# Kernel tuning notes

Hardware: AMD Instinct MI355X
Metric: run time of the kernel (lower is better)

Reference implementation:

```python
import jax, jax.numpy as jnp
import numpy as np

N_NODES = 100000
N_EDGES = 3200000
IN_CH = 256


def setup_inputs() -> dict:
    key = jax.random.key(0)
    ks = jax.random.split(key, 8)
    x = jax.random.normal(ks[0], (N_NODES, IN_CH), dtype=jnp.float32)
    edge_index = jax.random.randint(ks[1], (2, N_EDGES), 0, N_NODES, dtype=jnp.int64)
    alpha = jnp.ones((), dtype=jnp.float32)
    beta = jnp.ones((), dtype=jnp.float32)
    s = 1.0 / np.sqrt(IN_CH)
    W_mlp = jax.random.normal(ks[2], (1, IN_CH), dtype=jnp.float32) * s
    W_lin = jax.random.normal(ks[3], (1, IN_CH), dtype=jnp.float32) * s
    W_gcn = jax.random.normal(ks[4], (1, IN_CH), dtype=jnp.float32) * s
    W_att = jax.random.normal(ks[5], (3, 3), dtype=jnp.float32) * (1.0 / np.sqrt(3))
    b_att = jax.random.normal(ks[6], (3,), dtype=jnp.float32) * 0.1
    return {"x": x, "edge_index": edge_index, "alpha": alpha, "beta": beta,
            "W_mlp": W_mlp, "W_lin": W_lin, "W_gcn": W_gcn,
            "W_att": W_att, "b_att": b_att}


def _gcn_conv(x, edge_index, W_gcn, num_nodes):
    # PyG GCNConv: add self-loops, symmetric normalization, no bias.
    loop = jnp.arange(num_nodes, dtype=edge_index.dtype)
    row = jnp.concatenate([edge_index[0], loop])  # source
    col = jnp.concatenate([edge_index[1], loop])  # target
    deg = jax.ops.segment_sum(jnp.ones_like(col, dtype=x.dtype), col,
                              num_segments=num_nodes)
    dinv = jnp.where(deg > 0, jax.lax.rsqrt(deg), 0.0)
    norm = dinv[row] * dinv[col]                  # [E+N]
    xw = x @ W_gcn.T                               # [N, 1]
    msg = norm[:, None] * xw[row]                  # [E+N, 1]
    return jax.ops.segment_sum(msg, col, num_segments=num_nodes)  # [N, 1]


def reference(x, edge_index, alpha, beta, W_mlp, W_lin, W_gcn, W_att, b_att):
    num_nodes = x.shape[0]
    # score1: in-degree based
    deg = jax.ops.segment_sum(jnp.ones((edge_index.shape[1],), dtype=x.dtype),
                              edge_index[1], num_segments=num_nodes)
    score1 = jax.nn.sigmoid(alpha * jnp.sqrt(deg) + beta)           # [N]
    # score2: tiny MLP
    score2 = jax.nn.sigmoid((x @ W_mlp.T)[:, 0])                    # [N]
    # score3: GCNConv + linear
    gcn_out = _gcn_conv(x, edge_index, W_gcn, num_nodes)            # [N,1]
    score3 = jax.nn.sigmoid((gcn_out + x @ W_lin.T)[:, 0])          # [N]
    scores = jnp.stack([score1, score2, score3], axis=1)            # [N,3]
    weight = jax.nn.softmax(scores @ W_att.T + b_att, axis=1)       # [N,3]
    fitness = jnp.sum(weight * scores, axis=1)                      # [N]
    return fitness
```

## Files before the change

kernel.cpp:

```cpp
#include <hip/hip_runtime.h>
#include <math.h>

#define N_CH    256
#define SBSHIFT 11
#define SBN     2048
#define NSMAX   64
#define CH      4096


__device__ __forceinline__ float sigmoidf_(float v) {
    return 1.0f / (1.0f + expf(-v));
}

__device__ __forceinline__ void build_tables(const int* sbT, int ns,
                                             int* sbsL, int* cstL) {
    if (threadIdx.x == 0) {
        int run = 0, c = 0;
        for (int i = 0; i < ns; ++i) {
            sbsL[i] = run;
            cstL[i] = c;
            int len = sbT[i];
            run += len;
            c += (len + CH - 1) / CH;
        }
        sbsL[ns] = run;
        cstL[ns] = c;
    }
}

__global__ __launch_bounds__(256) void hist_kernel(
    const int* __restrict__ dst, int* __restrict__ H1,
    int n_edges, int ns, int nch)
{
    __shared__ int h8[NSMAX * 8];
    int c = blockIdx.x;
    for (int i = threadIdx.x; i < NSMAX * 8; i += 256) h8[i] = 0;
    __syncthreads();
    int copy = (int)threadIdx.x & 7;
    int start = c * CH;
    #pragma unroll
    for (int m = 0; m < 4; ++m) {
        int e = start + (m * 256 + (int)threadIdx.x) * 4;
        if (e + 3 < n_edges) {
            int4 d4 = *(const int4*)(dst + e);
            atomicAdd(&h8[(d4.x >> SBSHIFT) * 8 + copy], 1);
            atomicAdd(&h8[(d4.y >> SBSHIFT) * 8 + copy], 1);
            atomicAdd(&h8[(d4.z >> SBSHIFT) * 8 + copy], 1);
            atomicAdd(&h8[(d4.w >> SBSHIFT) * 8 + copy], 1);
        } else {
            for (int ee = e; ee < n_edges && ee >= 0; ++ee)
                atomicAdd(&h8[(dst[ee] >> SBSHIFT) * 8 + copy], 1);
        }
    }
    __syncthreads();
    if (threadIdx.x < (unsigned)ns) {
        int s = 0;
        #pragma unroll
        for (int k = 0; k < 8; ++k) s += h8[threadIdx.x * 8 + k];
        H1[(size_t)threadIdx.x * nch + c] = s;
    }
}

__global__ __launch_bounds__(1024) void scanA_kernel(
    const int* __restrict__ H1, int* __restrict__ O, int* __restrict__ sbT,
    int nch)
{
    __shared__ int s[1024];
    int sb = blockIdx.x, t = threadIdx.x;
    int v = (t < nch) ? H1[(size_t)sb * nch + t] : 0;
    s[t] = v;
    __syncthreads();
    for (int off = 1; off < 1024; off <<= 1) {
        int a = s[t];
        int b = (t >= off) ? s[t - off] : 0;
        __syncthreads();
        s[t] = a + b;
        __syncthreads();
    }
    if (t < nch) O[(size_t)sb * nch + t] = s[t] - v;
    if (t == 1023) sbT[sb] = s[1023];
}

__global__ __launch_bounds__(256) void scatter_dots_kernel(
    const int* __restrict__ src, const int* __restrict__ dst,
    const int* __restrict__ sbT, const int* __restrict__ O,
    const int* __restrict__ H1, int* __restrict__ cpack,
    const float* __restrict__ x,
    const float* __restrict__ Wmlp, const float* __restrict__ Wlin,
    const float* __restrict__ Wgcn,
    float* __restrict__ s2dot, float* __restrict__ s3lin, float* __restrict__ xw,
    int n_nodes, int n_edges, int ns, int nch)
{
    __shared__ int lp[NSMAX + 1];
    __shared__ int dl[NSMAX];
    __shared__ int h2[NSMAX];
    __shared__ unsigned short sbOf[CH];
    __shared__ int sorted[CH];

    int t = threadIdx.x;

    if ((int)blockIdx.x >= nch) {
        int wid  = ((int)blockIdx.x - nch) * 4 + (t >> 6);
        int lane = t & 63;
        if (wid >= n_nodes) return;

        const float4* xr = (const float4*)(x + (size_t)wid * N_CH);
        float4 v  = xr[lane];
        float4 wm = ((const float4*)Wmlp)[lane];
        float4 wl = ((const float4*)Wlin)[lane];
        float4 wg = ((const float4*)Wgcn)[lane];

        float d0 = v.x*wm.x + v.y*wm.y + v.z*wm.z + v.w*wm.w;
        float d1 = v.x*wl.x + v.y*wl.y + v.z*wl.z + v.w*wl.w;
        float d2 = v.x*wg.x + v.y*wg.y + v.z*wg.z + v.w*wg.w;

        #pragma unroll
        for (int off = 32; off; off >>= 1) {
            d0 += __shfl_down(d0, off, 64);
            d1 += __shfl_down(d1, off, 64);
            d2 += __shfl_down(d2, off, 64);
        }
        if (lane == 0) { s2dot[wid] = d0; s3lin[wid] = d1; xw[wid] = d2; }
        return;
    }

    int c = blockIdx.x;

    if (t < 64) {
        h2[t] = 0;
        int hv = (t < ns) ? H1[(size_t)t * nch + c] : 0;
        int sv = (t < ns) ? sbT[t] : 0;
        int hi = hv, si = sv;
        #pragma unroll
        for (int off = 1; off < 64; off <<= 1) {
            int a = __shfl_up(hi, off, 64); if (t >= off) hi += a;
            int b = __shfl_up(si, off, 64); if (t >= off) si += b;
        }
        if (t < ns) {
            int lpe = hi - hv;
            lp[t] = lpe;
            int sbs = si - sv;
            dl[t] = sbs + O[(size_t)t * nch + c] - lpe;
        }
        if (t == ns - 1) lp[ns] = hi;
    }
    __syncthreads();

    if (t < ns) {
        int p0 = lp[t], p1 = lp[t + 1];
        for (int p = p0; p < p1; ++p) sbOf[p] = (unsigned short)t;
    }

    int start = c * CH;
    int cnt = n_edges - start; if (cnt > CH) cnt = CH;

    #pragma unroll
    for (int m = 0; m < 4; ++m) {
        int e = start + (m * 256 + t) * 4;
        if (e + 3 < n_edges) {
            int4 s4 = *(const int4*)(src + e);
            int4 d4 = *(const int4*)(dst + e);
            int sb, r;
            sb = d4.x >> SBSHIFT; r = atomicAdd(&h2[sb], 1);
            sorted[lp[sb] + r] = s4.x | ((d4.x & (SBN - 1)) << 17);
            sb = d4.y >> SBSHIFT; r = atomicAdd(&h2[sb], 1);
            sorted[lp[sb] + r] = s4.y | ((d4.y & (SBN - 1)) << 17);
            sb = d4.z >> SBSHIFT; r = atomicAdd(&h2[sb], 1);
            sorted[lp[sb] + r] = s4.z | ((d4.z & (SBN - 1)) << 17);
            sb = d4.w >> SBSHIFT; r = atomicAdd(&h2[sb], 1);
            sorted[lp[sb] + r] = s4.w | ((d4.w & (SBN - 1)) << 17);
        } else {
            for (int j = 0; j < 4; ++j) {
                int ee = e + j;
                if (ee < n_edges && ee >= 0) {
                    int sv = src[ee], dv = dst[ee];
                    int sb = dv >> SBSHIFT;
                    int r = atomicAdd(&h2[sb], 1);
                    sorted[lp[sb] + r] = sv | ((dv & (SBN - 1)) << 17);
                }
            }
        }
    }
    __syncthreads();

    for (int p = t; p < cnt; p += 256) {
        cpack[dl[sbOf[p]] + p] = sorted[p];
    }
}

__global__ __launch_bounds__(256) void chunkDeg_kernel(
    const int* __restrict__ cpack, const int* __restrict__ sbT,
    int* __restrict__ partialD, int ns)
{
    __shared__ int sbsL[NSMAX + 1], cstL[NSMAX + 1];
    __shared__ int cnt[SBN];
    build_tables(sbT, ns, sbsL, cstL);
    for (int i = threadIdx.x; i < SBN; i += 256) cnt[i] = 0;
    __syncthreads();
    int c = blockIdx.x;
    if (c >= cstL[ns]) return;
    int lo = 0, hi = ns;
    while (hi - lo > 1) { int mid = (lo + hi) >> 1; if (cstL[mid] <= c) lo = mid; else hi = mid; }
    int sb = lo;
    int i0 = c - cstL[sb];
    int base = sbsL[sb] + i0 * CH;
    int len = sbsL[sb + 1] - base; if (len > CH) len = CH;

    #pragma unroll
    for (int m = 0; m < 4; ++m) {
        int e = (m * 256 + (int)threadIdx.x) * 4;
        if (e + 3 < len) {
            int4 w4 = *(const int4*)(cpack + base + e);
            atomicAdd(&cnt[w4.x >> 17], 1);
            atomicAdd(&cnt[w4.y >> 17], 1);
            atomicAdd(&cnt[w4.z >> 17], 1);
            atomicAdd(&cnt[w4.w >> 17], 1);
        } else {
            for (int ee = e; ee < len && ee >= 0; ++ee)
                atomicAdd(&cnt[cpack[base + ee] >> 17], 1);
        }
    }
    __syncthreads();
    int* row = partialD + (size_t)c * SBN;
    for (int i = threadIdx.x; i < SBN; i += 256) row[i] = cnt[i];
}

__global__ __launch_bounds__(256) void reduceDeg_kernel(
    const int* __restrict__ partialD, const int* __restrict__ sbT,
    const float* __restrict__ xw,
    float* __restrict__ degf, float* __restrict__ dinv, float* __restrict__ sxw,
    int n_nodes, int ns)
{
    __shared__ int sbsL[NSMAX + 1], cstL[NSMAX + 1];
    build_tables(sbT, ns, sbsL, cstL);
    __syncthreads();
    int i = blockIdx.x * 256 + threadIdx.x;
    if (i >= n_nodes) return;
    int sb = i >> SBSHIFT, li = i & (SBN - 1);
    int c0 = cstL[sb], c1 = cstL[sb + 1];
    int d = 0;
    for (int c = c0; c < c1; ++c) d += partialD[(size_t)c * SBN + li];
    float df = (float)d;
    degf[i] = df;
    float di = rsqrtf(df + 1.0f);
    dinv[i] = di;
    sxw[i]  = di * xw[i];
}

__global__ __launch_bounds__(256) void chunkAcc_kernel(
    const int* __restrict__ cpack, const int* __restrict__ sbT,
    const float* __restrict__ sxw, float* __restrict__ partialF, int ns)
{
    __shared__ int sbsL[NSMAX + 1], cstL[NSMAX + 1];
    __shared__ float facc[SBN];
    build_tables(sbT, ns, sbsL, cstL);
    for (int i = threadIdx.x; i < SBN; i += 256) facc[i] = 0.0f;
    __syncthreads();
    int c = blockIdx.x;
    if (c >= cstL[ns]) return;
    int lo = 0, hi = ns;
    while (hi - lo > 1) { int mid = (lo + hi) >> 1; if (cstL[mid] <= c) lo = mid; else hi = mid; }
    int sb = lo;
    int i0 = c - cstL[sb];
    int base = sbsL[sb] + i0 * CH;
    int len = sbsL[sb + 1] - base; if (len > CH) len = CH;

    #pragma unroll
    for (int m = 0; m < 4; ++m) {
        int e = (m * 256 + (int)threadIdx.x) * 4;
        if (e + 3 < len) {
            int4 w4 = *(const int4*)(cpack + base + e);
            atomicAdd(&facc[w4.x >> 17], sxw[w4.x & 0x1FFFF]);
            atomicAdd(&facc[w4.y >> 17], sxw[w4.y & 0x1FFFF]);
            atomicAdd(&facc[w4.z >> 17], sxw[w4.z & 0x1FFFF]);
            atomicAdd(&facc[w4.w >> 17], sxw[w4.w & 0x1FFFF]);
        } else {
            for (int ee = e; ee < len && ee >= 0; ++ee) {
                int w = cpack[base + ee];
                atomicAdd(&facc[w >> 17], sxw[w & 0x1FFFF]);
            }
        }
    }
    __syncthreads();
    float* row = partialF + (size_t)c * SBN;
    for (int i = threadIdx.x; i < SBN; i += 256) row[i] = facc[i];
}

__global__ __launch_bounds__(256) void reduceFinal_kernel(
    const float* __restrict__ partialF, const int* __restrict__ sbT,
    const float* __restrict__ degf, const float* __restrict__ dinv,
    const float* __restrict__ xw, const float* __restrict__ s2dot,
    const float* __restrict__ s3lin,
    const float* __restrict__ alpha, const float* __restrict__ beta,
    const float* __restrict__ Watt, const float* __restrict__ batt,
    float* __restrict__ out, int n_nodes, int ns)
{
    __shared__ int sbsL[NSMAX + 1], cstL[NSMAX + 1];
    build_tables(sbT, ns, sbsL, cstL);
    __syncthreads();
    int i = blockIdx.x * 256 + threadIdx.x;
    if (i >= n_nodes) return;
    int sb = i >> SBSHIFT, li = i & (SBN - 1);
    int c0 = cstL[sb], c1 = cstL[sb + 1];
    float acc = 0.0f;
    for (int c = c0; c < c1; ++c) acc += partialF[(size_t)c * SBN + li];

    float dn = dinv[i];
    float g  = acc * dn + dn * dn * xw[i];
    float s1 = sigmoidf_(alpha[0] * sqrtf(degf[i]) + beta[0]);
    float s2 = sigmoidf_(s2dot[i]);
    float s3 = sigmoidf_(g + s3lin[i]);

    float z0 = Watt[0]*s1 + Watt[1]*s2 + Watt[2]*s3 + batt[0];
    float z1 = Watt[3]*s1 + Watt[4]*s2 + Watt[5]*s3 + batt[1];
    float z2 = Watt[6]*s1 + Watt[7]*s2 + Watt[8]*s3 + batt[2];

    float m  = fmaxf(z0, fmaxf(z1, z2));
    float e0 = expf(z0 - m), e1 = expf(z1 - m), e2 = expf(z2 - m);
    float inv = 1.0f / (e0 + e1 + e2);
    out[i] = (e0 * s1 + e1 * s2 + e2 * s3) * inv;
}

extern "C" void kernel_launch(void* const* d_in, const int* in_sizes, int n_in,
                              void* d_out, int out_size, void* d_ws, size_t ws_size,
                              hipStream_t stream) {
    const float* x     = (const float*)d_in[0];
    const int*   ei    = (const int*)d_in[1];
    const float* alpha = (const float*)d_in[2];
    const float* beta  = (const float*)d_in[3];
    const float* Wmlp  = (const float*)d_in[4];
    const float* Wlin  = (const float*)d_in[5];
    const float* Wgcn  = (const float*)d_in[6];
    const float* Watt  = (const float*)d_in[7];
    const float* batt  = (const float*)d_in[8];
    float* out = (float*)d_out;

    int n_nodes = in_sizes[0] / N_CH;
    int n_edges = in_sizes[1] / 2;
    const int* src = ei;
    const int* dst = ei + n_edges;

    int ns  = (n_nodes + SBN - 1) >> SBSHIFT;
    int nch = (n_edges + CH - 1) / CH;
    int maxChunks = nch + ns;

    size_t off = 0;
    int*   cpack    = (int*)d_ws;          off += (((size_t)n_edges + 1023) & ~(size_t)1023);
    int*   H1       = (int*)d_ws + off;    off += (((size_t)ns * nch + 1023) & ~(size_t)1023);
    int*   O        = (int*)d_ws + off;    off += (((size_t)ns * nch + 1023) & ~(size_t)1023);
    int*   sbT      = (int*)d_ws + off;    off += 128;
    int*   partialD = (int*)d_ws + off;    off += (size_t)maxChunks * SBN;
    float* partialF = (float*)d_ws + off;  off += (size_t)maxChunks * SBN;
    float* s2dot    = (float*)d_ws + off;  off += (((size_t)n_nodes + 1023) & ~(size_t)1023);
    float* s3lin    = (float*)d_ws + off;  off += (((size_t)n_nodes + 1023) & ~(size_t)1023);
    float* xw       = (float*)d_ws + off;  off += (((size_t)n_nodes + 1023) & ~(size_t)1023);
    float* degf     = (float*)d_ws + off;  off += (((size_t)n_nodes + 1023) & ~(size_t)1023);
    float* dinv     = (float*)d_ws + off;  off += (((size_t)n_nodes + 1023) & ~(size_t)1023);
    float* sxw      = (float*)d_ws + off;  off += (((size_t)n_nodes + 1023) & ~(size_t)1023);

    hist_kernel<<<nch, 256, 0, stream>>>(dst, H1, n_edges, ns, nch);

    scanA_kernel<<<ns, 1024, 0, stream>>>(H1, O, sbT, nch);

    int dotsBlocks = (n_nodes + 3) / 4;
    scatter_dots_kernel<<<nch + dotsBlocks, 256, 0, stream>>>(
        src, dst, sbT, O, H1, cpack,
        x, Wmlp, Wlin, Wgcn, s2dot, s3lin, xw,
        n_nodes, n_edges, ns, nch);

    chunkDeg_kernel<<<maxChunks, 256, 0, stream>>>(cpack, sbT, partialD, ns);

    reduceDeg_kernel<<<(n_nodes + 255) / 256, 256, 0, stream>>>(
        partialD, sbT, xw, degf, dinv, sxw, n_nodes, ns);

    chunkAcc_kernel<<<maxChunks, 256, 0, stream>>>(cpack, sbT, sxw, partialF, ns);

    reduceFinal_kernel<<<(n_nodes + 255) / 256, 256, 0, stream>>>(
        partialF, sbT, degf, dinv, xw, s2dot, s3lin,
        alpha, beta, Watt, batt, out, n_nodes, ns);
}
```

Before: 233.9 us.

## Replace global histogram and scan with fixed-capacity superblock slots and atomic counters

```diff
diff --git a/kernel.cpp b/kernel.cpp
--- a/kernel.cpp
+++ b/kernel.cpp
@@ -6,94 +6,26 @@
 #define SBN     2048
 #define NSMAX   64
 #define CH      4096
+#define SLOTS   20
+#define CAP     (SLOTS * CH)
 
 
 __device__ __forceinline__ float sigmoidf_(float v) {
     return 1.0f / (1.0f + expf(-v));
 }
 
-__device__ __forceinline__ void build_tables(const int* sbT, int ns,
-                                             int* sbsL, int* cstL) {
-    if (threadIdx.x == 0) {
-        int run = 0, c = 0;
-        for (int i = 0; i < ns; ++i) {
-            sbsL[i] = run;
-            cstL[i] = c;
-            int len = sbT[i];
-            run += len;
-            c += (len + CH - 1) / CH;
-        }
-        sbsL[ns] = run;
-        cstL[ns] = c;
-    }
-}
-
-__global__ __launch_bounds__(256) void hist_kernel(
-    const int* __restrict__ dst, int* __restrict__ H1,
-    int n_edges, int ns, int nch)
-{
-    __shared__ int h8[NSMAX * 8];
-    int c = blockIdx.x;
-    for (int i = threadIdx.x; i < NSMAX * 8; i += 256) h8[i] = 0;
-    __syncthreads();
-    int copy = (int)threadIdx.x & 7;
-    int start = c * CH;
-    #pragma unroll
-    for (int m = 0; m < 4; ++m) {
-        int e = start + (m * 256 + (int)threadIdx.x) * 4;
-        if (e + 3 < n_edges) {
-            int4 d4 = *(const int4*)(dst + e);
-            atomicAdd(&h8[(d4.x >> SBSHIFT) * 8 + copy], 1);
-            atomicAdd(&h8[(d4.y >> SBSHIFT) * 8 + copy], 1);
-            atomicAdd(&h8[(d4.z >> SBSHIFT) * 8 + copy], 1);
-            atomicAdd(&h8[(d4.w >> SBSHIFT) * 8 + copy], 1);
-        } else {
-            for (int ee = e; ee < n_edges && ee >= 0; ++ee)
-                atomicAdd(&h8[(dst[ee] >> SBSHIFT) * 8 + copy], 1);
-        }
-    }
-    __syncthreads();
-    if (threadIdx.x < (unsigned)ns) {
-        int s = 0;
-        #pragma unroll
-        for (int k = 0; k < 8; ++k) s += h8[threadIdx.x * 8 + k];
-        H1[(size_t)threadIdx.x * nch + c] = s;
-    }
-}
-
-__global__ __launch_bounds__(1024) void scanA_kernel(
-    const int* __restrict__ H1, int* __restrict__ O, int* __restrict__ sbT,
-    int nch)
-{
-    __shared__ int s[1024];
-    int sb = blockIdx.x, t = threadIdx.x;
-    int v = (t < nch) ? H1[(size_t)sb * nch + t] : 0;
-    s[t] = v;
-    __syncthreads();
-    for (int off = 1; off < 1024; off <<= 1) {
-        int a = s[t];
-        int b = (t >= off) ? s[t - off] : 0;
-        __syncthreads();
-        s[t] = a + b;
-        __syncthreads();
-    }
-    if (t < nch) O[(size_t)sb * nch + t] = s[t] - v;
-    if (t == 1023) sbT[sb] = s[1023];
-}
-
 __global__ __launch_bounds__(256) void scatter_dots_kernel(
     const int* __restrict__ src, const int* __restrict__ dst,
-    const int* __restrict__ sbT, const int* __restrict__ O,
-    const int* __restrict__ H1, int* __restrict__ cpack,
+    int* __restrict__ gcnt, int* __restrict__ cpack,
     const float* __restrict__ x,
     const float* __restrict__ Wmlp, const float* __restrict__ Wlin,
     const float* __restrict__ Wgcn,
     float* __restrict__ s2dot, float* __restrict__ s3lin, float* __restrict__ xw,
     int n_nodes, int n_edges, int ns, int nch)
 {
+    __shared__ int h[NSMAX];
     __shared__ int lp[NSMAX + 1];
     __shared__ int dl[NSMAX];
-    __shared__ int h2[NSMAX];
     __shared__ unsigned short sbOf[CH];
     __shared__ int sorted[CH];
 
@@ -125,86 +57,95 @@
     }
 
     int c = blockIdx.x;
-
-    if (t < 64) {
-        h2[t] = 0;
-        int hv = (t < ns) ? H1[(size_t)t * nch + c] : 0;
-        int sv = (t < ns) ? sbT[t] : 0;
-        int hi = hv, si = sv;
-        #pragma unroll
-        for (int off = 1; off < 64; off <<= 1) {
-            int a = __shfl_up(hi, off, 64); if (t >= off) hi += a;
-            int b = __shfl_up(si, off, 64); if (t >= off) si += b;
-        }
-        if (t < ns) {
-            int lpe = hi - hv;
-            lp[t] = lpe;
-            int sbs = si - sv;
-            dl[t] = sbs + O[(size_t)t * nch + c] - lpe;
-        }
-        if (t == ns - 1) lp[ns] = hi;
-    }
-    __syncthreads();
-
-    if (t < ns) {
-        int p0 = lp[t], p1 = lp[t + 1];
-        for (int p = p0; p < p1; ++p) sbOf[p] = (unsigned short)t;
-    }
+    if (t < NSMAX) h[t] = 0;
+    __syncthreads();
 
     int start = c * CH;
     int cnt = n_edges - start; if (cnt > CH) cnt = CH;
 
+    int4 s4[4], d4[4];
     #pragma unroll
     for (int m = 0; m < 4; ++m) {
         int e = start + (m * 256 + t) * 4;
         if (e + 3 < n_edges) {
-            int4 s4 = *(const int4*)(src + e);
-            int4 d4 = *(const int4*)(dst + e);
-            int sb, r;
-            sb = d4.x >> SBSHIFT; r = atomicAdd(&h2[sb], 1);
-            sorted[lp[sb] + r] = s4.x | ((d4.x & (SBN - 1)) << 17);
-            sb = d4.y >> SBSHIFT; r = atomicAdd(&h2[sb], 1);
-            sorted[lp[sb] + r] = s4.y | ((d4.y & (SBN - 1)) << 17);
-            sb = d4.z >> SBSHIFT; r = atomicAdd(&h2[sb], 1);
-            sorted[lp[sb] + r] = s4.z | ((d4.z & (SBN - 1)) << 17);
-            sb = d4.w >> SBSHIFT; r = atomicAdd(&h2[sb], 1);
-            sorted[lp[sb] + r] = s4.w | ((d4.w & (SBN - 1)) << 17);
+            s4[m] = *(const int4*)(src + e);
+            d4[m] = *(const int4*)(dst + e);
+            atomicAdd(&h[d4[m].x >> SBSHIFT], 1);
+            atomicAdd(&h[d4[m].y >> SBSHIFT], 1);
+            atomicAdd(&h[d4[m].z >> SBSHIFT], 1);
+            atomicAdd(&h[d4[m].w >> SBSHIFT], 1);
         } else {
+            s4[m] = make_int4(-1, -1, -1, -1);
+            int* sp = (int*)&s4[m]; int* dp = (int*)&d4[m];
             for (int j = 0; j < 4; ++j) {
                 int ee = e + j;
                 if (ee < n_edges && ee >= 0) {
-                    int sv = src[ee], dv = dst[ee];
-                    int sb = dv >> SBSHIFT;
-                    int r = atomicAdd(&h2[sb], 1);
-                    sorted[lp[sb] + r] = sv | ((dv & (SBN - 1)) << 17);
+                    sp[j] = src[ee]; dp[j] = dst[ee];
+                    atomicAdd(&h[dp[j] >> SBSHIFT], 1);
                 }
             }
         }
     }
     __syncthreads();
 
+    if (t < 64) {
+        int hv = (t < ns) ? h[t] : 0;
+        int hi = hv;
+        #pragma unroll
+        for (int off = 1; off < 64; off <<= 1) {
+            int a = __shfl_up(hi, off, 64); if (t >= off) hi += a;
+        }
+        if (t < ns) {
+            int lpe = hi - hv;
+            lp[t] = lpe;
+            int base = hv ? atomicAdd(&gcnt[t], hv) : 0;
+            dl[t] = t * CAP + base - lpe;
+        }
+        if (t == ns - 1) lp[ns] = hi;
+    }
+    __syncthreads();
+
+    if (t < ns) {
+        int p0 = lp[t], p1 = lp[t + 1];
+        for (int p = p0; p < p1; ++p) sbOf[p] = (unsigned short)t;
+    }
+    if (t < NSMAX) h[t] = 0;
+    __syncthreads();
+
+    #pragma unroll
+    for (int m = 0; m < 4; ++m) {
+        int* sp = (int*)&s4[m]; int* dp = (int*)&d4[m];
+        #pragma unroll
+        for (int j = 0; j < 4; ++j) {
+            if (sp[j] >= 0) {
+                int d = dp[j];
+                int sb = d >> SBSHIFT;
+                int r = atomicAdd(&h[sb], 1);
+                sorted[lp[sb] + r] = sp[j] | ((d & (SBN - 1)) << 17);
+            }
+        }
+    }
+    __syncthreads();
+
     for (int p = t; p < cnt; p += 256) {
         cpack[dl[sbOf[p]] + p] = sorted[p];
     }
 }
 
 __global__ __launch_bounds__(256) void chunkDeg_kernel(
-    const int* __restrict__ cpack, const int* __restrict__ sbT,
-    int* __restrict__ partialD, int ns)
-{
-    __shared__ int sbsL[NSMAX + 1], cstL[NSMAX + 1];
+    const int* __restrict__ cpack, const int* __restrict__ gcnt,
+    int* __restrict__ partialD)
+{
+    int c = blockIdx.x;
+    int sb = c / SLOTS, slot = c - sb * SLOTS;
+    int len = gcnt[sb] - slot * CH;
+    if (len <= 0) return;
+    if (len > CH) len = CH;
+
     __shared__ int cnt[SBN];
-    build_tables(sbT, ns, sbsL, cstL);
     for (int i = threadIdx.x; i < SBN; i += 256) cnt[i] = 0;
     __syncthreads();
-    int c = blockIdx.x;
-    if (c >= cstL[ns]) return;
-    int lo = 0, hi = ns;
-    while (hi - lo > 1) { int mid = (lo + hi) >> 1; if (cstL[mid] <= c) lo = mid; else hi = mid; }
-    int sb = lo;
-    int i0 = c - cstL[sb];
-    int base = sbsL[sb] + i0 * CH;
-    int len = sbsL[sb + 1] - base; if (len > CH) len = CH;
+    int base = sb * CAP + slot * CH;
 
     #pragma unroll
     for (int m = 0; m < 4; ++m) {
@@ -226,20 +167,18 @@
 }
 
 __global__ __launch_bounds__(256) void reduceDeg_kernel(
-    const int* __restrict__ partialD, const int* __restrict__ sbT,
+    const int* __restrict__ partialD, const int* __restrict__ gcnt,
     const float* __restrict__ xw,
     float* __restrict__ degf, float* __restrict__ dinv, float* __restrict__ sxw,
-    int n_nodes, int ns)
-{
-    __shared__ int sbsL[NSMAX + 1], cstL[NSMAX + 1];
-    build_tables(sbT, ns, sbsL, cstL);
-    __syncthreads();
+    int n_nodes)
+{
     int i = blockIdx.x * 256 + threadIdx.x;
     if (i >= n_nodes) return;
     int sb = i >> SBSHIFT, li = i & (SBN - 1);
-    int c0 = cstL[sb], c1 = cstL[sb + 1];
+    int nsl = (gcnt[sb] + CH - 1) / CH; if (nsl > SLOTS) nsl = SLOTS;
     int d = 0;
-    for (int c = c0; c < c1; ++c) d += partialD[(size_t)c * SBN + li];
+    for (int s = 0; s < nsl; ++s)
+        d += partialD[((size_t)sb * SLOTS + s) * SBN + li];
     float df = (float)d;
     degf[i] = df;
     float di = rsqrtf(df + 1.0f);
@@ -248,22 +187,19 @@
 }
 
 __global__ __launch_bounds__(256) void chunkAcc_kernel(
-    const int* __restrict__ cpack, const int* __restrict__ sbT,
-    const float* __restrict__ sxw, float* __restrict__ partialF, int ns)
-{
-    __shared__ int sbsL[NSMAX + 1], cstL[NSMAX + 1];
+    const int* __restrict__ cpack, const int* __restrict__ gcnt,
+    const float* __restrict__ sxw, float* __restrict__ partialF)
+{
+    int c = blockIdx.x;
+    int sb = c / SLOTS, slot = c - sb * SLOTS;
+    int len = gcnt[sb] - slot * CH;
+    if (len <= 0) return;
+    if (len > CH) len = CH;
+
     __shared__ float facc[SBN];
-    build_tables(sbT, ns, sbsL, cstL);
     for (int i = threadIdx.x; i < SBN; i += 256) facc[i] = 0.0f;
     __syncthreads();
-    int c = blockIdx.x;
-    if (c >= cstL[ns]) return;
-    int lo = 0, hi = ns;
-    while (hi - lo > 1) { int mid = (lo + hi) >> 1; if (cstL[mid] <= c) lo = mid; else hi = mid; }
-    int sb = lo;
-    int i0 = c - cstL[sb];
-    int base = sbsL[sb] + i0 * CH;
-    int len = sbsL[sb + 1] - base; if (len > CH) len = CH;
+    int base = sb * CAP + slot * CH;
 
     #pragma unroll
     for (int m = 0; m < 4; ++m) {
@@ -287,23 +223,21 @@
 }
 
 __global__ __launch_bounds__(256) void reduceFinal_kernel(
-    const float* __restrict__ partialF, const int* __restrict__ sbT,
+    const float* __restrict__ partialF, const int* __restrict__ gcnt,
     const float* __restrict__ degf, const float* __restrict__ dinv,
     const float* __restrict__ xw, const float* __restrict__ s2dot,
     const float* __restrict__ s3lin,
     const float* __restrict__ alpha, const float* __restrict__ beta,
     const float* __restrict__ Watt, const float* __restrict__ batt,
-    float* __restrict__ out, int n_nodes, int ns)
-{
-    __shared__ int sbsL[NSMAX + 1], cstL[NSMAX + 1];
-    build_tables(sbT, ns, sbsL, cstL);
-    __syncthreads();
+    float* __restrict__ out, int n_nodes)
+{
     int i = blockIdx.x * 256 + threadIdx.x;
     if (i >= n_nodes) return;
     int sb = i >> SBSHIFT, li = i & (SBN - 1);
-    int c0 = cstL[sb], c1 = cstL[sb + 1];
+    int nsl = (gcnt[sb] + CH - 1) / CH; if (nsl > SLOTS) nsl = SLOTS;
     float acc = 0.0f;
-    for (int c = c0; c < c1; ++c) acc += partialF[(size_t)c * SBN + li];
+    for (int s = 0; s < nsl; ++s)
+        acc += partialF[((size_t)sb * SLOTS + s) * SBN + li];
 
     float dn = dinv[i];
     float g  = acc * dn + dn * dn * xw[i];
@@ -342,15 +276,12 @@
 
     int ns  = (n_nodes + SBN - 1) >> SBSHIFT;
     int nch = (n_edges + CH - 1) / CH;
-    int maxChunks = nch + ns;
 
     size_t off = 0;
-    int*   cpack    = (int*)d_ws;          off += (((size_t)n_edges + 1023) & ~(size_t)1023);
-    int*   H1       = (int*)d_ws + off;    off += (((size_t)ns * nch + 1023) & ~(size_t)1023);
-    int*   O        = (int*)d_ws + off;    off += (((size_t)ns * nch + 1023) & ~(size_t)1023);
-    int*   sbT      = (int*)d_ws + off;    off += 128;
-    int*   partialD = (int*)d_ws + off;    off += (size_t)maxChunks * SBN;
-    float* partialF = (float*)d_ws + off;  off += (size_t)maxChunks * SBN;
+    int*   cpack    = (int*)d_ws;          off += (((size_t)ns * CAP + 1023) & ~(size_t)1023);
+    int*   gcnt     = (int*)d_ws + off;    off += 128;
+    int*   partialD = (int*)d_ws + off;    off += (size_t)ns * SLOTS * SBN;
+    float* partialF = (float*)d_ws + off;  off += (size_t)ns * SLOTS * SBN;
     float* s2dot    = (float*)d_ws + off;  off += (((size_t)n_nodes + 1023) & ~(size_t)1023);
     float* s3lin    = (float*)d_ws + off;  off += (((size_t)n_nodes + 1023) & ~(size_t)1023);
     float* xw       = (float*)d_ws + off;  off += (((size_t)n_nodes + 1023) & ~(size_t)1023);
@@ -358,24 +289,22 @@
     float* dinv     = (float*)d_ws + off;  off += (((size_t)n_nodes + 1023) & ~(size_t)1023);
     float* sxw      = (float*)d_ws + off;  off += (((size_t)n_nodes + 1023) & ~(size_t)1023);
 
-    hist_kernel<<<nch, 256, 0, stream>>>(dst, H1, n_edges, ns, nch);
-
-    scanA_kernel<<<ns, 1024, 0, stream>>>(H1, O, sbT, nch);
+    hipMemsetAsync(gcnt, 0, NSMAX * sizeof(int), stream);
 
     int dotsBlocks = (n_nodes + 3) / 4;
     scatter_dots_kernel<<<nch + dotsBlocks, 256, 0, stream>>>(
-        src, dst, sbT, O, H1, cpack,
+        src, dst, gcnt, cpack,
         x, Wmlp, Wlin, Wgcn, s2dot, s3lin, xw,
         n_nodes, n_edges, ns, nch);
 
-    chunkDeg_kernel<<<maxChunks, 256, 0, stream>>>(cpack, sbT, partialD, ns);
+    chunkDeg_kernel<<<ns * SLOTS, 256, 0, stream>>>(cpack, gcnt, partialD);
 
     reduceDeg_kernel<<<(n_nodes + 255) / 256, 256, 0, stream>>>(
-        partialD, sbT, xw, degf, dinv, sxw, n_nodes, ns);
-
-    chunkAcc_kernel<<<maxChunks, 256, 0, stream>>>(cpack, sbT, sxw, partialF, ns);
+        partialD, gcnt, xw, degf, dinv, sxw, n_nodes);
+
+    chunkAcc_kernel<<<ns * SLOTS, 256, 0, stream>>>(cpack, gcnt, sxw, partialF);
 
     reduceFinal_kernel<<<(n_nodes + 255) / 256, 256, 0, stream>>>(
-        partialF, sbT, degf, dinv, xw, s2dot, s3lin,
-        alpha, beta, Watt, batt, out, n_nodes, ns);
-}
+        partialF, gcnt, degf, dinv, xw, s2dot, s3lin,
+        alpha, beta, Watt, batt, out, n_nodes);
+}
```

After: 238.5 us. About the same (+2.0%).
